# Optimization experiments

Hardware: AMD Instinct MI355X
Metric: run time of the kernel (lower is better)

The kernel has to match this reference:

```python
import jax, jax.numpy as jnp
import numpy as np

B, C, L, NLAB, EMB, NFREQ, D = 256, 64, 512, 10, 256, 9, 8
FIN, FH, FOUT = 4 * C, C, C
P_TOTAL = FIN * FH + FH + FH * FOUT + FOUT + FIN * FOUT + FOUT


def _leaky(x):
    return jax.nn.leaky_relu(x, 0.2)


def _conv1d(x, w, b=None, pad=0):
    y = jax.lax.conv_general_dilated(x, w, (1,), [(pad, pad)], dimension_numbers=('NCH', 'OIH', 'NCH'))
    return y if b is None else y + b[None, :, None]


def _res1d(x, w0, b0, w1, b1, ws=None, pad=1):
    # GAN-stability style residual block: out = shortcut(x) + 0.1 * conv1(act(conv0(act(x))))
    xs = _conv1d(x, ws) if ws is not None else x
    dx = _conv1d(_leaky(x), w0, b0, pad)
    dx = _conv1d(_leaky(dx), w1, b1, pad)
    return xs + 0.1 * dx


def _pos_enc():
    # sinusoidal positional encoding, 2*NFREQ channels over L positions
    p = np.arange(L, dtype=np.float32)
    f = (np.pi / 2.0 ** np.arange(NFREQ, dtype=np.float32))[:, None]
    pe = np.concatenate([np.sin(f * p), np.cos(f * p)], axis=0)  # [2*NFREQ, L]
    return jnp.asarray(pe)


def _sobel_kernels():
    s = np.array([1.0, 2.0, 1.0], np.float32)
    d = np.array([-1.0, 0.0, 1.0], np.float32)
    kx = np.einsum('i,j,k->ijk', d, s, s)
    ky = np.einsum('i,j,k->ijk', s, d, s)
    kz = np.einsum('i,j,k->ijk', s, s, d)
    return jnp.asarray(np.stack([kx, ky, kz]))  # [3, 3, 3, 3]


def _sin_sobel(x, k):
    # depthwise 3D sobel along each axis, sin of gradients, concat with input -> 4C channels
    outs = [x]
    for i in range(3):
        w = jnp.broadcast_to(k[i][None, None], (C, 1, 3, 3, 3))
        g = jax.lax.conv_general_dilated(x, w, (1, 1, 1), [(1, 1)] * 3,
                                         dimension_numbers=('NCDHW', 'OIDHW', 'NCDHW'),
                                         feature_group_count=C)
        outs.append(jnp.sin(g))
    return jnp.concatenate(outs, axis=1)


def _inst_norm(x):
    m = x.mean(axis=(2, 3, 4), keepdims=True)
    v = x.var(axis=(2, 3, 4), keepdims=True)
    return (x - m) * jax.lax.rsqrt(v + 1e-5)


def _dyna(x, p):
    # hypernet-generated per-sample 1x1x1 residual conv block
    b = x.shape[0]
    xf = x.reshape(b, FIN, D * D * D)
    o = FIN * FH
    wh = p[:, :o].reshape(b, FH, FIN)
    bh = p[:, o:o + FH]; o += FH
    wl = p[:, o:o + FH * FOUT].reshape(b, FOUT, FH); o += FH * FOUT
    bl = p[:, o:o + FOUT]; o += FOUT
    ws = p[:, o:o + FIN * FOUT].reshape(b, FOUT, FIN); o += FIN * FOUT
    bs = p[:, o:o + FOUT]
    xs = jnp.einsum('boi,bis->bos', ws, xf) + bs[:, :, None]
    dx = _leaky(jnp.einsum('bhi,bis->bhs', wh, xf) + bh[:, :, None])
    dx = jnp.einsum('boh,bhs->bos', wl, dx) + bl[:, :, None]
    return (xs + 0.1 * dx).reshape(b, FOUT, D, D, D)


def _forward(codes, y, fc_w, fc_b, in_w0, in_b0, in_w1, in_b1, in_ws, leak, hyper_w, hyper_b,
             out_w0, out_b0, out_w1, out_b1, l1_w0, l1_b0, l1_w1, l1_b1,
             l2_w0, l2_b0, l2_w1, l2_b1, l2_ws):
    b = codes.shape[0]
    yemb = jax.nn.one_hot(y, NLAB, dtype=codes.dtype) @ fc_w.T + fc_b
    yemb = yemb / jnp.maximum(jnp.linalg.norm(yemb, axis=1, keepdims=True), 1e-12)
    pe = jnp.broadcast_to(_pos_enc()[None], (b, 2 * NFREQ, L))
    x = jnp.concatenate([codes, pe], axis=1)  # [B, C+2*NFREQ, L]
    x = _res1d(x, in_w0, in_b0, in_w1, in_b1, ws=in_ws)
    x = x.reshape(b, C, D, D, D)
    leak_c = jnp.clip(leak, 0.001, 1000.0)
    p = yemb @ hyper_w.T + hyper_b  # per-sample dynamic conv params [B, P_TOTAL]
    k = _sobel_kernels()
    for _ in range(8):
        xn = _inst_norm(x)
        xn = _sin_sobel(xn, k)
        xn = _dyna(xn, p)
        x = x + leak_c * xn
    x = x.reshape(b, C, L)
    x = _res1d(x, out_w0, out_b0, out_w1, out_b1)
    code_idx = jnp.argmax(codes, axis=1).reshape(b * L)
    logits = x.transpose(0, 2, 1).reshape(b * L, C)
    logp = jax.nn.log_softmax(logits, axis=-1)
    loss_cent = -jnp.take_along_axis(logp, code_idx[:, None], axis=1).mean()
    lat = _res1d(x, l1_w0, l1_b0, l1_w1, l1_b1, pad=0)
    lat = _res1d(lat, l2_w0, l2_b0, l2_w1, l2_b1, ws=l2_ws, pad=0)
    return lat[:, 0, :], loss_cent


def setup_inputs() -> dict:
    key = jax.random.key(0)
    ks = jax.random.split(key, 16)
    w = lambda k, s: 0.02 * jax.random.normal(k, s, jnp.float32)
    z = lambda s: jnp.zeros(s, jnp.float32)
    CIN = C + 2 * NFREQ  # 82
    return {
        'codes': jax.random.normal(ks[0], (B, C, L), jnp.float32),
        'y': jax.random.randint(ks[1], (B,), 0, NLAB),
        'fc_w': w(ks[2], (EMB, NLAB)), 'fc_b': z((EMB,)),
        'in_w0': w(ks[3], (C, CIN, 3)), 'in_b0': z((C,)),
        'in_w1': w(ks[4], (C, C, 3)), 'in_b1': z((C,)),
        'in_ws': w(ks[5], (C, CIN, 1)),
        'leak': jnp.asarray(0.1, jnp.float32),
        'hyper_w': w(ks[6], (P_TOTAL, EMB)), 'hyper_b': z((P_TOTAL,)),
        'out_w0': w(ks[7], (C, C, 3)), 'out_b0': z((C,)),
        'out_w1': w(ks[8], (C, C, 3)), 'out_b1': z((C,)),
        'l1_w0': w(ks[9], (C, C, 1)), 'l1_b0': z((C,)),
        'l1_w1': w(ks[10], (C, C, 1)), 'l1_b1': z((C,)),
        'l2_w0': w(ks[11], (1, C, 1)), 'l2_b0': z((1,)),
        'l2_w1': w(ks[12], (1, 1, 1)), 'l2_b1': z((1,)),
        'l2_ws': w(ks[13], (1, C, 1)),
    }


def reference(codes, y, fc_w, fc_b, in_w0, in_b0, in_w1, in_b1, in_ws, leak, hyper_w, hyper_b,
              out_w0, out_b0, out_w1, out_b1, l1_w0, l1_b0, l1_w1, l1_b1,
              l2_w0, l2_b0, l2_w1, l2_b1, l2_ws):
    return _forward(codes, y, fc_w, fc_b, in_w0, in_b0, in_w1, in_b1, in_ws, leak, hyper_w, hyper_b,
                    out_w0, out_b0, out_w1, out_b1, l1_w0, l1_b0, l1_w1, l1_b1,
                    l2_w0, l2_b0, l2_w1, l2_b1, l2_ws)
```

## Files before the change

### kernel.cpp

```cpp
#include <hip/hip_runtime.h>

#define B_ 256
#define C_ 64
#define L_ 512
#define CIN_ 82
#define NFREQ_ 9
#define EMB_ 256
#define NLAB_ 10
#define PT_ 37056
#define OFF_BH 16384
#define OFF_WL 16448
#define OFF_BL 20544
#define OFF_WS 20608
#define OFF_BS 36992
#define PI_F 3.14159265358979323846f

typedef short bh8 __attribute__((ext_vector_type(8)));
typedef float f32x4 __attribute__((ext_vector_type(4)));

__device__ inline float lrelu(float v){ return v > 0.f ? v : 0.2f*v; }

__device__ inline unsigned short f2bf(float f){
  unsigned u = __float_as_uint(f);
  u += 0x7FFFu + ((u >> 16) & 1u);
  return (unsigned short)(u >> 16);
}
__device__ inline float bf2f(unsigned short u){
  return __uint_as_float((unsigned)u << 16);
}
__device__ inline unsigned pk2(float a, float b){
  return (unsigned)f2bf(a) | ((unsigned)f2bf(b) << 16);
}
__device__ inline bh8 cvt8(float4 a, float4 b){
  bh8 r;
  r[0]=(short)f2bf(a.x); r[1]=(short)f2bf(a.y); r[2]=(short)f2bf(a.z); r[3]=(short)f2bf(a.w);
  r[4]=(short)f2bf(b.x); r[5]=(short)f2bf(b.y); r[6]=(short)f2bf(b.z); r[7]=(short)f2bf(b.w);
  return r;
}
__device__ inline void ld8(const float* p, float* d){
  float4 a = *(const float4*)p, b = *(const float4*)(p + 4);
  d[0]=a.x; d[1]=a.y; d[2]=a.z; d[3]=a.w; d[4]=b.x; d[5]=b.y; d[6]=b.z; d[7]=b.w;
}
__device__ inline void st8(float* p, const float* s){
  float4 a = {s[0],s[1],s[2],s[3]}, b = {s[4],s[5],s[6],s[7]};
  *(float4*)p = a; *(float4*)(p + 4) = b;
}
__device__ inline uint4 pk8(const float* v){
  uint4 o = { pk2(v[0],v[1]), pk2(v[2],v[3]), pk2(v[4],v[5]), pk2(v[6],v[7]) };
  return o;
}

__global__ __launch_bounds__(256) void k_yemb(const float* __restrict__ fc_w,
    const float* __restrict__ fc_b, const int* __restrict__ y,
    unsigned short* __restrict__ ybf, float* __restrict__ out){
  int b = blockIdx.x, e = threadIdx.x;
  int lab = y[b];
  float v = fc_w[e*NLAB_ + lab] + fc_b[e];
  __shared__ float red[256];
  red[e] = v*v; __syncthreads();
  for (int s = 128; s; s >>= 1){ if (e < s) red[e] += red[e+s]; __syncthreads(); }
  float nrm = fmaxf(sqrtf(red[0]), 1e-12f);
  ybf[(size_t)b*EMB_ + e] = f2bf(v / nrm);
  if (b == 0 && e == 0) out[B_*L_] = 0.f;
}

__global__ __launch_bounds__(256) void k_hyper(const float* __restrict__ hw,
    const float* __restrict__ hb, const unsigned short* __restrict__ ybf,
    unsigned short* __restrict__ p_bf){
  int tid = threadIdx.x;
  int wid = tid >> 6, lane = tid & 63, col = lane & 15, quad = lane >> 4;
  int j = blockIdx.x*64 + wid*16 + col;
  f32x4 acc[16];
  f32x4 z4 = {0.f,0.f,0.f,0.f};
  #pragma unroll
  for (int i = 0; i < 16; i++) acc[i] = z4;
  for (int k0 = 0; k0 < 256; k0 += 32){
    const float* hp = hw + (size_t)j*EMB_ + k0 + quad*8;
    bh8 bf = cvt8(*(const float4*)hp, *(const float4*)(hp+4));
    #pragma unroll
    for (int mt = 0; mt < 16; mt++){
      bh8 af = *(const bh8*)&ybf[(size_t)(mt*16 + col)*EMB_ + k0 + quad*8];
      acc[mt] = __builtin_amdgcn_mfma_f32_16x16x32_bf16(af, bf, acc[mt], 0, 0, 0);
    }
  }
  float hbv = hb[j];
  #pragma unroll
  for (int mt = 0; mt < 16; mt++){
    int b0 = mt*16 + quad*4;
    #pragma unroll
    for (int r = 0; r < 4; r++)
      p_bf[(size_t)(b0 + r)*PT_ + j] = f2bf(acc[mt][r] + hbv);
  }
}

__device__ inline float pe_raw(int fi, int l){
  if (fi < NFREQ_) return __sinf(PI_F / (float)(1 << fi) * (float)l);
  return __cosf(PI_F / (float)(1 << (fi - NFREQ_)) * (float)l);
}

__global__ __launch_bounds__(256) void k_conv_in1(const float* __restrict__ codes,
    const float* __restrict__ w0, const float* __restrict__ b0,
    unsigned short* __restrict__ t1bf){
  int b = blockIdx.x, l0 = blockIdx.y*128, tid = threadIdx.x;
  int wid = tid>>6, lane = tid&63, col = lane&15, quad = lane>>4;
  __shared__ __attribute__((aligned(16))) unsigned short xT[136][96];
  __shared__ __attribute__((aligned(16))) unsigned short wA[3][64][96];
  for (int i = tid; i < 64*96; i += 256){
    int m = i / 96, cin = i % 96;
    if (cin < CIN_){
      const float* s = w0 + (size_t)m*(CIN_*3) + cin*3;
      wA[0][m][cin] = f2bf(s[0]); wA[1][m][cin] = f2bf(s[1]); wA[2][m][cin] = f2bf(s[2]);
    } else { wA[0][m][cin] = 0; wA[1][m][cin] = 0; wA[2][m][cin] = 0; }
  }
  const float* cb = codes + (size_t)b*C_*L_;
  for (int i = tid; i < 96*34; i += 256){
    int c = i / 34, g = i % 34;
    int lg = l0 - 4 + 4*g;
    #pragma unroll
    for (int r2 = 0; r2 < 4; r2++){
      int l = lg + r2;
      float xv = 0.f;
      if (l >= 0 && l < L_){
        if (c < C_) xv = cb[(size_t)c*L_ + l];
        else if (c < CIN_) xv = pe_raw(c - C_, l);
      }
      xT[4*g + r2][c] = f2bf(lrelu(xv));
    }
  }
  __syncthreads();
  f32x4 z4 = {0.f,0.f,0.f,0.f};
  f32x4 acc[8];
  #pragma unroll
  for (int i = 0; i < 8; i++) acc[i] = z4;
  #pragma unroll
  for (int t = 0; t < 3; t++){
    #pragma unroll
    for (int k0 = 0; k0 < 96; k0 += 32){
      bh8 bfr[2];
      #pragma unroll
      for (int nt = 0; nt < 2; nt++)
        bfr[nt] = *(const bh8*)&xT[wid*32 + nt*16 + col + t + 3][k0 + quad*8];
      #pragma unroll
      for (int mt = 0; mt < 4; mt++){
        bh8 af = *(const bh8*)&wA[t][mt*16 + col][k0 + quad*8];
        #pragma unroll
        for (int nt = 0; nt < 2; nt++)
          acc[mt*2+nt] = __builtin_amdgcn_mfma_f32_16x16x32_bf16(af, bfr[nt], acc[mt*2+nt], 0,0,0);
      }
    }
  }
  #pragma unroll
  for (int mt = 0; mt < 4; mt++){
    int f0 = mt*16 + quad*4;
    float q0 = b0[f0], q1 = b0[f0+1], q2 = b0[f0+2], q3 = b0[f0+3];
    #pragma unroll
    for (int nt = 0; nt < 2; nt++){
      int l = l0 + wid*32 + nt*16 + col;
      f32x4 a = acc[mt*2+nt];
      uint2 o = { pk2(lrelu(a[0]+q0), lrelu(a[1]+q1)),
                  pk2(lrelu(a[2]+q2), lrelu(a[3]+q3)) };
      *(uint2*)&t1bf[((size_t)b*L_ + l)*64 + f0] = o;
    }
  }
}

__global__ __launch_bounds__(256) void k_conv_in2(const float* __restrict__ codes,
    const float* __restrict__ wsp, const float* __restrict__ w1, const float* __restrict__ b1,
    const unsigned short* __restrict__ t1bf, float* __restrict__ x){
  int b = blockIdx.x, l0 = blockIdx.y*128, tid = threadIdx.x;
  int wid = tid>>6, lane = tid&63, col = lane&15, quad = lane>>4;
  __shared__ __attribute__((aligned(16))) unsigned short xT[128][96];
  __shared__ __attribute__((aligned(16))) unsigned short wsA[64][96];
  __shared__ __attribute__((aligned(16))) unsigned short w1A[3][64][72];
  for (int i = tid; i < 64*96; i += 256){
    int m = i / 96, cin = i % 96;
    wsA[m][cin] = (cin < CIN_) ? f2bf(wsp[(size_t)m*CIN_ + cin]) : (unsigned short)0;
  }
  for (int i = tid; i < 64*64; i += 256){
    int m = i >> 6, cin = i & 63;
    const float* s = w1 + (size_t)m*192 + cin*3;
    w1A[0][m][cin] = f2bf(s[0]); w1A[1][m][cin] = f2bf(s[1]); w1A[2][m][cin] = f2bf(s[2]);
  }
  const float* cb = codes + (size_t)b*C_*L_;
  for (int i = tid; i < 96*32; i += 256){
    int c = i / 32, g = i % 32;
    int lg = l0 + 4*g;
    #pragma unroll
    for (int r2 = 0; r2 < 4; r2++){
      int l = lg + r2;
      float xv;
      if (c < C_) xv = cb[(size_t)c*L_ + l];
      else if (c < CIN_) xv = pe_raw(c - C_, l);
      else xv = 0.f;
      xT[4*g + r2][c] = f2bf(xv);
    }
  }
  __syncthreads();
  f32x4 z4 = {0.f,0.f,0.f,0.f};
  f32x4 accS[8], accD[8];
  #pragma unroll
  for (int i = 0; i < 8; i++){ accS[i] = z4; accD[i] = z4; }
  #pragma unroll
  for (int k0 = 0; k0 < 96; k0 += 32){
    bh8 bfr[2];
    #pragma unroll
    for (int nt = 0; nt < 2; nt++)
      bfr[nt] = *(const bh8*)&xT[wid*32 + nt*16 + col][k0 + quad*8];
    #pragma unroll
    for (int mt = 0; mt < 4; mt++){
      bh8 af = *(const bh8*)&wsA[mt*16 + col][k0 + quad*8];
      #pragma unroll
      for (int nt = 0; nt < 2; nt++)
        accS[mt*2+nt] = __builtin_amdgcn_mfma_f32_16x16x32_bf16(af, bfr[nt], accS[mt*2+nt], 0,0,0);
    }
  }
  bh8 zz8 = {0,0,0,0,0,0,0,0};
  #pragma unroll
  for (int t = 0; t < 3; t++){
    #pragma unroll
    for (int k0 = 0; k0 < 64; k0 += 32){
      bh8 bfr[2];
      #pragma unroll
      for (int nt = 0; nt < 2; nt++){
        int l = l0 + wid*32 + nt*16 + col + t - 1;
        bfr[nt] = (l >= 0 && l < L_)
          ? *(const bh8*)&t1bf[((size_t)b*L_ + l)*64 + k0 + quad*8] : zz8;
      }
      #pragma unroll
      for (int mt = 0; mt < 4; mt++){
        bh8 af = *(const bh8*)&w1A[t][mt*16 + col][k0 + quad*8];
        #pragma unroll
        for (int nt = 0; nt < 2; nt++)
          accD[mt*2+nt] = __builtin_amdgcn_mfma_f32_16x16x32_bf16(af, bfr[nt], accD[mt*2+nt], 0,0,0);
      }
    }
  }
  #pragma unroll
  for (int mt = 0; mt < 4; mt++){
    int f0 = mt*16 + quad*4;
    float q0 = b1[f0], q1 = b1[f0+1], q2 = b1[f0+2], q3 = b1[f0+3];
    #pragma unroll
    for (int nt = 0; nt < 2; nt++){
      int l = l0 + wid*32 + nt*16 + col;
      f32x4 s = accS[mt*2+nt], d = accD[mt*2+nt];
      size_t base = ((size_t)b*C_ + f0)*L_ + l;
      x[base]        = s[0] + 0.1f*(d[0] + q0);
      x[base + L_]   = s[1] + 0.1f*(d[1] + q1);
      x[base + 2*L_] = s[2] + 0.1f*(d[2] + q2);
      x[base + 3*L_] = s[3] + 0.1f*(d[3] + q3);
    }
  }
}

#define TGS 4144
#define TBS (4*TGS)
__global__ __launch_bounds__(512, 2) void k_loop(float* __restrict__ x,
    const unsigned short* __restrict__ p_bf, const float* __restrict__ leak){
  const int b = blockIdx.x, tid = threadIdx.x;
  const int wid = tid >> 6, lane = tid & 63, col = lane & 15, quad = lane >> 4;
  const int yy = lane & 7, zz = lane >> 3;
  const unsigned short* pb = p_bf + (size_t)b*PT_;
  float* xb = x + (size_t)b*C_*L_;

  __shared__ __attribute__((aligned(16))) char sm_raw[81920 + 2*TBS*2];
  float (*S)[64][8] = (float (*)[64][8])(sm_raw + (size_t)wid*(5*64*8*4));
  unsigned short (*h_t)[72] = (unsigned short (*)[72])sm_raw;
  unsigned short* Tb = (unsigned short*)(sm_raw + 81920);

  const int lm = (yy > 0) ? lane-1 : lane;  const float wm = (yy > 0) ? 1.f : 0.f;
  const int lp = (yy < 7) ? lane+1 : lane;  const float wp = (yy < 7) ? 1.f : 0.f;
  const int zm = (zz > 0) ? lane-8 : lane;  const float qm = (zz > 0) ? 1.f : 0.f;
  const int zp = (zz < 7) ? lane+8 : lane;  const float qp = (zz < 7) ? 1.f : 0.f;

  const float lk = fminf(fmaxf(leak[0], 0.001f), 1000.f);
  const int base_t = wid*512 + lane*8;
  const f32x4 z4 = {0.f,0.f,0.f,0.f};

  for (int it = 0; it < 8; ++it){
    f32x4 acc_h[16], acc_s[16];
    #pragma unroll
    for (int i = 0; i < 16; i++){ acc_h[i] = z4; acc_s[i] = z4; }
    const float* xr0 = xb + (size_t)wid*L_ + lane*8;
    float4 nv0 = *(const float4*)xr0, nv1 = *(const float4*)(xr0 + 4);
    for (int cc = 0; cc < 8; ++cc){
      unsigned short* Tc = Tb + (cc & 1)*TBS;
      float r[8] = {nv0.x,nv0.y,nv0.z,nv0.w,nv1.x,nv1.y,nv1.z,nv1.w};
      if (cc < 7){
        const float* xr = xb + (size_t)((cc+1)*8 + wid)*L_ + lane*8;
        nv0 = *(const float4*)xr; nv1 = *(const float4*)(xr + 4);
      }
      float s1 = 0.f, s2 = 0.f;
      #pragma unroll
      for (int i = 0; i < 8; i++){ s1 += r[i]; s2 += r[i]*r[i]; }
      #pragma unroll
      for (int m = 32; m; m >>= 1){ s1 += __shfl_xor(s1, m); s2 += __shfl_xor(s2, m); }
      const float mean = s1 * (1.f/512.f);
      const float rstd = rsqrtf(s2*(1.f/512.f) - mean*mean + 1e-5f);
      float xn[8];
      #pragma unroll
      for (int i = 0; i < 8; i++) xn[i] = (r[i]-mean)*rstd;
      *(uint4*)&Tc[base_t] = pk8(xn);
      float A[8], Bv[8];
      A[0] = 2.f*xn[0]+xn[1]; Bv[0] = xn[1];
      #pragma unroll
      for (int i = 1; i < 7; i++){ A[i] = xn[i-1]+2.f*xn[i]+xn[i+1]; Bv[i] = xn[i+1]-xn[i-1]; }
      A[7] = xn[6]+2.f*xn[7]; Bv[7] = -xn[6];
      st8(&S[0][lane][0], A); st8(&S[1][lane][0], Bv);
      __syncthreads();
      float Cv[8], Dv[8], Ev[8];
      { float am[8], ap[8];
        ld8(&S[0][lm][0], am); ld8(&S[0][lp][0], ap);
        #pragma unroll
        for (int i = 0; i < 8; i++){ float a_m = am[i]*wm, a_p = ap[i]*wp;
          Cv[i] = a_m + 2.f*A[i] + a_p; Dv[i] = a_p - a_m; }
        ld8(&S[1][lm][0], am); ld8(&S[1][lp][0], ap);
        #pragma unroll
        for (int i = 0; i < 8; i++) Ev[i] = am[i]*wm + 2.f*Bv[i] + ap[i]*wp;
      }
      st8(&S[2][lane][0], Cv); st8(&S[3][lane][0], Dv); st8(&S[4][lane][0], Ev);
      __syncthreads();
      { float um[8], up[8], sg[8];
        ld8(&S[2][zm][0], um); ld8(&S[2][zp][0], up);
        #pragma unroll
        for (int i = 0; i < 8; i++) sg[i] = __sinf(up[i]*qp - um[i]*qm);
        *(uint4*)&Tc[TGS + base_t] = pk8(sg);
        ld8(&S[3][zm][0], um); ld8(&S[3][zp][0], up);
        #pragma unroll
        for (int i = 0; i < 8; i++) sg[i] = __sinf(um[i]*qm + 2.f*Dv[i] + up[i]*qp);
        *(uint4*)&Tc[2*TGS + base_t] = pk8(sg);
        ld8(&S[4][zm][0], um); ld8(&S[4][zp][0], up);
        #pragma unroll
        for (int i = 0; i < 8; i++) sg[i] = __sinf(um[i]*qm + 2.f*Ev[i] + up[i]*qp);
        *(uint4*)&Tc[3*TGS + base_t] = pk8(sg);
      }
      __syncthreads();
      bh8 bfr[4];
      #pragma unroll
      for (int nt = 0; nt < 4; nt++){
        const int n = wid*64 + nt*16 + col;
        bh8 fv;
        #pragma unroll
        for (int j = 0; j < 8; j++) fv[j] = (short)Tc[quad*TGS + j*512 + n];
        bfr[nt] = fv;
      }
      #pragma unroll
      for (int mt = 0; mt < 4; mt++){
        const int m = mt*16 + col;
        bh8 ah = *(const bh8*)&pb[(size_t)m*256 + quad*64 + cc*8];
        bh8 aw = *(const bh8*)&pb[OFF_WS + (size_t)m*256 + quad*64 + cc*8];
        #pragma unroll
        for (int nt = 0; nt < 4; nt++){
          acc_h[mt*4+nt] = __builtin_amdgcn_mfma_f32_16x16x32_bf16(ah, bfr[nt], acc_h[mt*4+nt], 0,0,0);
          acc_s[mt*4+nt] = __builtin_amdgcn_mfma_f32_16x16x32_bf16(aw, bfr[nt], acc_s[mt*4+nt], 0,0,0);
        }
      }
    }
    #pragma unroll
    for (int mt = 0; mt < 4; mt++){
      const int f0 = mt*16 + quad*4;
      const float bh0 = bf2f(pb[OFF_BH+f0]),   bh1 = bf2f(pb[OFF_BH+f0+1]);
      const float bh2 = bf2f(pb[OFF_BH+f0+2]), bh3 = bf2f(pb[OFF_BH+f0+3]);
      #pragma unroll
      for (int nt = 0; nt < 4; nt++){
        const int n = wid*64 + nt*16 + col;
        f32x4 a = acc_h[mt*4+nt];
        uint2 o = { pk2(lrelu(a[0]+bh0), lrelu(a[1]+bh1)),
                    pk2(lrelu(a[2]+bh2), lrelu(a[3]+bh3)) };
        *(uint2*)&h_t[n][f0] = o;
      }
    }
    __syncthreads();
    f32x4 acc2[16];
    #pragma unroll
    for (int i = 0; i < 16; i++) acc2[i] = z4;
    #pragma unroll
    for (int k0 = 0; k0 < 64; k0 += 32){
      bh8 hb[4];
      #pragma unroll
      for (int nt = 0; nt < 4; nt++)
        hb[nt] = *(const bh8*)&h_t[wid*64 + nt*16 + col][k0 + quad*8];
      #pragma unroll
      for (int mt = 0; mt < 4; mt++){
        bh8 al = *(const bh8*)&pb[OFF_WL + (size_t)(mt*16 + col)*64 + k0 + quad*8];
        #pragma unroll
        for (int nt = 0; nt < 4; nt++)
          acc2[mt*4+nt] = __builtin_amdgcn_mfma_f32_16x16x32_bf16(al, hb[nt], acc2[mt*4+nt], 0,0,0);
      }
    }
    #pragma unroll
    for (int mt = 0; mt < 4; mt++){
      const int f0 = mt*16 + quad*4;
      const float bs0 = bf2f(pb[OFF_BS+f0]),   bs1 = bf2f(pb[OFF_BS+f0+1]);
      const float bs2 = bf2f(pb[OFF_BS+f0+2]), bs3 = bf2f(pb[OFF_BS+f0+3]);
      const float bl0 = bf2f(pb[OFF_BL+f0]),   bl1 = bf2f(pb[OFF_BL+f0+1]);
      const float bl2 = bf2f(pb[OFF_BL+f0+2]), bl3 = bf2f(pb[OFF_BL+f0+3]);
      #pragma unroll
      for (int nt = 0; nt < 4; nt++){
        const int n = wid*64 + nt*16 + col;
        f32x4 xs = acc_s[mt*4+nt], dx = acc2[mt*4+nt];
        size_t xi = (size_t)f0*L_ + n;
        xb[xi]        += lk*(xs[0] + bs0 + 0.1f*(dx[0] + bl0));
        xb[xi + L_]   += lk*(xs[1] + bs1 + 0.1f*(dx[1] + bl1));
        xb[xi + 2*L_] += lk*(xs[2] + bs2 + 0.1f*(dx[2] + bl2));
        xb[xi + 3*L_] += lk*(xs[3] + bs3 + 0.1f*(dx[3] + bl3));
      }
    }
    __threadfence_block();
    __syncthreads();
  }
}

__global__ __launch_bounds__(256) void k_conv_out1(const float* __restrict__ x,
    const float* __restrict__ w, const float* __restrict__ bias,
    unsigned short* __restrict__ t1bf){
  int b = blockIdx.x, l0 = blockIdx.y*128, tid = threadIdx.x;
  int wid = tid>>6, lane = tid&63, col = lane&15, quad = lane>>4;
  __shared__ __attribute__((aligned(16))) unsigned short xT[136][72];
  __shared__ __attribute__((aligned(16))) unsigned short wA[3][64][72];
  for (int i = tid; i < 64*64; i += 256){
    int m = i >> 6, cin = i & 63;
    const float* s = w + (size_t)m*192 + cin*3;
    wA[0][m][cin] = f2bf(s[0]); wA[1][m][cin] = f2bf(s[1]); wA[2][m][cin] = f2bf(s[2]);
  }
  const float* xb = x + (size_t)b*C_*L_;
  for (int i = tid; i < 64*34; i += 256){
    int c = i / 34, g = i % 34;
    int lg = l0 - 4 + 4*g;
    if (lg >= 0 && lg + 3 < L_){
      float4 f = *(const float4*)&xb[(size_t)c*L_ + lg];
      xT[4*g  ][c] = f2bf(lrelu(f.x));
      xT[4*g+1][c] = f2bf(lrelu(f.y));
      xT[4*g+2][c] = f2bf(lrelu(f.z));
      xT[4*g+3][c] = f2bf(lrelu(f.w));
    } else {
      #pragma unroll
      for (int r2 = 0; r2 < 4; r2++){
        int l = lg + r2;
        float v = (l >= 0 && l < L_) ? xb[(size_t)c*L_ + l] : 0.f;
        xT[4*g + r2][c] = f2bf(lrelu(v));
      }
    }
  }
  __syncthreads();
  f32x4 z4 = {0.f,0.f,0.f,0.f};
  f32x4 acc[8];
  #pragma unroll
  for (int i = 0; i < 8; i++) acc[i] = z4;
  #pragma unroll
  for (int t = 0; t < 3; t++){
    #pragma unroll
    for (int k0 = 0; k0 < 64; k0 += 32){
      bh8 bfr[2];
      #pragma unroll
      for (int nt = 0; nt < 2; nt++)
        bfr[nt] = *(const bh8*)&xT[wid*32 + nt*16 + col + t + 3][k0 + quad*8];
      #pragma unroll
      for (int mt = 0; mt < 4; mt++){
        bh8 af = *(const bh8*)&wA[t][mt*16 + col][k0 + quad*8];
        #pragma unroll
        for (int nt = 0; nt < 2; nt++)
          acc[mt*2+nt] = __builtin_amdgcn_mfma_f32_16x16x32_bf16(af, bfr[nt], acc[mt*2+nt], 0,0,0);
      }
    }
  }
  #pragma unroll
  for (int mt = 0; mt < 4; mt++){
    int f0 = mt*16 + quad*4;
    float q0 = bias[f0], q1 = bias[f0+1], q2 = bias[f0+2], q3 = bias[f0+3];
    #pragma unroll
    for (int nt = 0; nt < 2; nt++){
      int l = l0 + wid*32 + nt*16 + col;
      f32x4 a = acc[mt*2+nt];
      uint2 o = { pk2(lrelu(a[0]+q0), lrelu(a[1]+q1)),
                  pk2(lrelu(a[2]+q2), lrelu(a[3]+q3)) };
      *(uint2*)&t1bf[((size_t)b*L_ + l)*64 + f0] = o;
    }
  }
}

__global__ __launch_bounds__(256) void k_conv_out2(float* __restrict__ x,
    const unsigned short* __restrict__ t1bf, const float* __restrict__ w,
    const float* __restrict__ bias){
  int b = blockIdx.x, l0 = blockIdx.y*256, tid = threadIdx.x;
  int wid = tid>>6, lane = tid&63, col = lane&15, quad = lane>>4;
  __shared__ __attribute__((aligned(16))) unsigned short wA[3][64][72];
  for (int i = tid; i < 64*64; i += 256){
    int m = i >> 6, cin = i & 63;
    const float* s = w + (size_t)m*192 + cin*3;
    wA[0][m][cin] = f2bf(s[0]); wA[1][m][cin] = f2bf(s[1]); wA[2][m][cin] = f2bf(s[2]);
  }
  __syncthreads();
  f32x4 z4 = {0.f,0.f,0.f,0.f};
  f32x4 acc[16];
  #pragma unroll
  for (int i = 0; i < 16; i++) acc[i] = z4;
  bh8 zz8 = {0,0,0,0,0,0,0,0};
  #pragma unroll
  for (int t = 0; t < 3; t++){
    #pragma unroll
    for (int k0 = 0; k0 < 64; k0 += 32){
      bh8 bfr[4];
      #pragma unroll
      for (int nt = 0; nt < 4; nt++){
        int l = l0 + wid*64 + nt*16 + col + t - 1;
        bfr[nt] = (l >= 0 && l < L_)
          ? *(const bh8*)&t1bf[((size_t)b*L_ + l)*64 + k0 + quad*8] : zz8;
      }
      #pragma unroll
      for (int mt = 0; mt < 4; mt++){
        bh8 af = *(const bh8*)&wA[t][mt*16 + col][k0 + quad*8];
        #pragma unroll
        for (int nt = 0; nt < 4; nt++)
          acc[mt*4+nt] = __builtin_amdgcn_mfma_f32_16x16x32_bf16(af, bfr[nt], acc[mt*4+nt], 0,0,0);
      }
    }
  }
  #pragma unroll
  for (int mt = 0; mt < 4; mt++){
    int f0 = mt*16 + quad*4;
    float q0 = bias[f0], q1 = bias[f0+1], q2 = bias[f0+2], q3 = bias[f0+3];
    #pragma unroll
    for (int nt = 0; nt < 4; nt++){
      int l = l0 + wid*64 + nt*16 + col;
      f32x4 a = acc[mt*4+nt];
      size_t base = ((size_t)b*C_ + f0)*L_ + l;
      x[base]        += 0.1f*(a[0] + q0);
      x[base + L_]   += 0.1f*(a[1] + q1);
      x[base + 2*L_] += 0.1f*(a[2] + q2);
      x[base + 3*L_] += 0.1f*(a[3] + q3);
    }
  }
}

__global__ __launch_bounds__(256) void k_loss(const float* __restrict__ x,
    const float* __restrict__ codes, float* __restrict__ out){
  int b = blockIdx.x;
  int l = blockIdx.y*256 + threadIdx.x;
  const float* xb = x + (size_t)b*C_*L_ + l;
  const float* cb = codes + (size_t)b*C_*L_ + l;
  float m = -1e30f, cm = -1e30f;
  int ci = 0;
  for (int c = 0; c < C_; c++){
    float xv = xb[(size_t)c*L_];
    m = fmaxf(m, xv);
    float cv = cb[(size_t)c*L_];
    if (cv > cm){ cm = cv; ci = c; }
  }
  float s = 0.f, vi = 0.f;
  for (int c = 0; c < C_; c++){
    float xv = xb[(size_t)c*L_];
    s += expf(xv - m);
    if (c == ci) vi = xv;
  }
  float lp = vi - m - logf(s);
  __shared__ float red[256];
  red[threadIdx.x] = -lp; __syncthreads();
  for (int sft = 128; sft; sft >>= 1){
    if (threadIdx.x < sft) red[threadIdx.x] += red[threadIdx.x + sft];
    __syncthreads();
  }
  if (threadIdx.x == 0) atomicAdd(out + B_*L_, red[0] * (1.0f/131072.0f));
}

__global__ __launch_bounds__(256) void k_lat(const float* __restrict__ x,
    const float* __restrict__ w10, const float* __restrict__ b10,
    const float* __restrict__ w11, const float* __restrict__ b11,
    const float* __restrict__ w20, const float* __restrict__ b20,
    const float* __restrict__ w21, const float* __restrict__ b21,
    const float* __restrict__ ws2, float* __restrict__ out){
  int b = blockIdx.x, l0 = blockIdx.y*256;
  int tid = threadIdx.x;
  int wid = tid >> 6, lane = tid & 63, col = lane & 15, quad = lane >> 4;
  __shared__ __attribute__((aligned(16))) unsigned short wA[2][64][72];
  __shared__ __attribute__((aligned(16))) unsigned short Bt[256][72];

  for (int i = tid; i < 1024; i += 256){
    int arr = i >> 9, rem = i & 511, row = rem >> 3, seg = rem & 7;
    const float* src = (arr ? w11 : w10) + (size_t)row*C_ + seg*8;
    *(bh8*)&wA[arr][row][seg*8] = cvt8(*(const float4*)src, *(const float4*)(src+4));
  }
  for (int i = tid; i < 4096; i += 256){
    int c = i >> 6, seg = i & 63;
    float4 v = *(const float4*)&x[((size_t)b*C_ + c)*L_ + l0 + seg*4];
    Bt[seg*4+0][c] = f2bf(lrelu(v.x));
    Bt[seg*4+1][c] = f2bf(lrelu(v.y));
    Bt[seg*4+2][c] = f2bf(lrelu(v.z));
    Bt[seg*4+3][c] = f2bf(lrelu(v.w));
  }
  __syncthreads();
  f32x4 z4 = {0.f,0.f,0.f,0.f};
  f32x4 acc1[16];
  #pragma unroll
  for (int i = 0; i < 16; i++) acc1[i] = z4;
  #pragma unroll
  for (int k0 = 0; k0 < 64; k0 += 32){
    bh8 bfr[4];
    #pragma unroll
    for (int nt = 0; nt < 4; nt++)
      bfr[nt] = *(const bh8*)&Bt[wid*64 + nt*16 + col][k0 + quad*8];
    #pragma unroll
    for (int mt = 0; mt < 4; mt++){
      bh8 af = *(const bh8*)&wA[0][mt*16 + col][k0 + quad*8];
      #pragma unroll
      for (int nt = 0; nt < 4; nt++)
        acc1[mt*4+nt] = __builtin_amdgcn_mfma_f32_16x16x32_bf16(af, bfr[nt], acc1[mt*4+nt], 0, 0, 0);
    }
  }
  #pragma unroll
  for (int mt = 0; mt < 4; mt++){
    int f0 = mt*16 + quad*4;
    f32x4 bv = *(const f32x4*)&b10[f0];
    #pragma unroll
    for (int nt = 0; nt < 4; nt++){
      int n = wid*64 + nt*16 + col;
      f32x4 a = acc1[mt*4+nt];
      uint2 o = { pk2(lrelu(a[0]+bv[0]), lrelu(a[1]+bv[1])),
                  pk2(lrelu(a[2]+bv[2]), lrelu(a[3]+bv[3])) };
      *(uint2*)&Bt[n][f0] = o;
    }
  }
  f32x4 acc2[16];
  #pragma unroll
  for (int i = 0; i < 16; i++) acc2[i] = z4;
  #pragma unroll
  for (int k0 = 0; k0 < 64; k0 += 32){
    bh8 bfr[4];
    #pragma unroll
    for (int nt = 0; nt < 4; nt++)
      bfr[nt] = *(const bh8*)&Bt[wid*64 + nt*16 + col][k0 + quad*8];
    #pragma unroll
    for (int mt = 0; mt < 4; mt++){
      bh8 af = *(const bh8*)&wA[1][mt*16 + col][k0 + quad*8];
      #pragma unroll
      for (int nt = 0; nt < 4; nt++)
        acc2[mt*4+nt] = __builtin_amdgcn_mfma_f32_16x16x32_bf16(af, bfr[nt], acc2[mt*4+nt], 0, 0, 0);
    }
  }
  float psA[4] = {0.f,0.f,0.f,0.f}, psB[4] = {0.f,0.f,0.f,0.f};
  #pragma unroll
  for (int mt = 0; mt < 4; mt++){
    int f0 = mt*16 + quad*4;
    f32x4 b11v = *(const f32x4*)&b11[f0];
    f32x4 wsv  = *(const f32x4*)&ws2[f0];
    f32x4 w20v = *(const f32x4*)&w20[f0];
    #pragma unroll
    for (int nt = 0; nt < 4; nt++){
      int lg = l0 + wid*64 + nt*16 + col;
      size_t base = ((size_t)b*C_ + f0)*L_ + lg;
      f32x4 a = acc2[mt*4+nt];
      #pragma unroll
      for (int r = 0; r < 4; r++){
        float xv = x[base + (size_t)r*L_];
        float lat = xv + 0.1f*(a[r] + b11v[r]);
        psA[nt] += wsv[r]*lat;
        psB[nt] += w20v[r]*lrelu(lat);
      }
    }
  }
  #pragma unroll
  for (int nt = 0; nt < 4; nt++){
    psA[nt] += __shfl_xor(psA[nt], 16); psA[nt] += __shfl_xor(psA[nt], 32);
    psB[nt] += __shfl_xor(psB[nt], 16); psB[nt] += __shfl_xor(psB[nt], 32);
  }
  if (quad == 0){
    float b20s = b20[0], w21s = w21[0], b21s = b21[0];
    #pragma unroll
    for (int nt = 0; nt < 4; nt++){
      float dx2 = w21s*lrelu(psB[nt] + b20s) + b21s;
      out[(size_t)b*L_ + l0 + wid*64 + nt*16 + col] = psA[nt] + 0.1f*dx2;
    }
  }
}

extern "C" void kernel_launch(void* const* d_in, const int* in_sizes, int n_in,
                              void* d_out, int out_size, void* d_ws, size_t ws_size,
                              hipStream_t stream) {
  (void)in_sizes; (void)n_in; (void)out_size; (void)ws_size;
  const float* codes   = (const float*)d_in[0];
  const int*   y       = (const int*)  d_in[1];
  const float* fc_w    = (const float*)d_in[2];
  const float* fc_b    = (const float*)d_in[3];
  const float* in_w0   = (const float*)d_in[4];
  const float* in_b0   = (const float*)d_in[5];
  const float* in_w1   = (const float*)d_in[6];
  const float* in_b1   = (const float*)d_in[7];
  const float* in_wsp  = (const float*)d_in[8];
  const float* leak    = (const float*)d_in[9];
  const float* hyper_w = (const float*)d_in[10];
  const float* hyper_b = (const float*)d_in[11];
  const float* out_w0  = (const float*)d_in[12];
  const float* out_b0  = (const float*)d_in[13];
  const float* out_w1  = (const float*)d_in[14];
  const float* out_b1  = (const float*)d_in[15];
  const float* l1_w0   = (const float*)d_in[16];
  const float* l1_b0   = (const float*)d_in[17];
  const float* l1_w1   = (const float*)d_in[18];
  const float* l1_b1   = (const float*)d_in[19];
  const float* l2_w0   = (const float*)d_in[20];
  const float* l2_b0   = (const float*)d_in[21];
  const float* l2_w1   = (const float*)d_in[22];
  const float* l2_b1   = (const float*)d_in[23];
  const float* l2_ws   = (const float*)d_in[24];
  float* out = (float*)d_out;

  char* ws = (char*)d_ws;
  unsigned short* p_bf = (unsigned short*)(ws);
  unsigned short* ybf  = (unsigned short*)(ws + 18972672);
  float* x             = (float*)(ws + 19103744);
  unsigned short* t1bf = (unsigned short*)(ws + 52658176);

  k_yemb<<<B_, 256, 0, stream>>>(fc_w, fc_b, y, ybf, out);
  k_hyper<<<PT_/64, 256, 0, stream>>>(hyper_w, hyper_b, ybf, p_bf);
  k_conv_in1<<<dim3(B_, 4), 256, 0, stream>>>(codes, in_w0, in_b0, t1bf);
  k_conv_in2<<<dim3(B_, 4), 256, 0, stream>>>(codes, in_wsp, in_w1, in_b1, t1bf, x);
  k_loop<<<B_, 512, 0, stream>>>(x, p_bf, leak);
  k_conv_out1<<<dim3(B_, 4), 256, 0, stream>>>(x, out_w0, out_b0, t1bf);
  k_conv_out2<<<dim3(B_, 2), 256, 0, stream>>>(x, t1bf, out_w1, out_b1);
  k_loss<<<dim3(B_, 2), 256, 0, stream>>>(x, codes, out);
  k_lat<<<dim3(B_, 2), 256, 0, stream>>>(x, l1_w0, l1_b0, l1_w1, l1_b1,
                                         l2_w0, l2_b0, l2_w1, l2_b1, l2_ws, out);
}
```

Baseline: 856.6 us.

## Batch 32 channels per sync and use bpermute shuffles for Sobel stencil

In k_loop, the instance-norm and Sobel stage now processes 32 channels per half before one barrier and one MFMA burst, instead of syncing three times per 8-channel chunk. The y/z neighbour exchange for the separable Sobel uses ds_bpermute cross-lane shuffles instead of staging through per-wave shared-memory scratch. The hyper and shortcut accumulators are merged into one 32-tile array, and the barrier after writing h_t is removed because each wave reads only its own rows. The intent is to cut barrier stalls and LDS round-trips. In exchange it issues many more per-dword permutes, and the larger live accumulator set raises register pressure.

```diff
diff --git a/kernel.cpp b/kernel.cpp
--- a/kernel.cpp
+++ b/kernel.cpp
@@ -37,17 +37,12 @@
   r[4]=(short)f2bf(b.x); r[5]=(short)f2bf(b.y); r[6]=(short)f2bf(b.z); r[7]=(short)f2bf(b.w);
   return r;
 }
-__device__ inline void ld8(const float* p, float* d){
-  float4 a = *(const float4*)p, b = *(const float4*)(p + 4);
-  d[0]=a.x; d[1]=a.y; d[2]=a.z; d[3]=a.w; d[4]=b.x; d[5]=b.y; d[6]=b.z; d[7]=b.w;
-}
-__device__ inline void st8(float* p, const float* s){
-  float4 a = {s[0],s[1],s[2],s[3]}, b = {s[4],s[5],s[6],s[7]};
-  *(float4*)p = a; *(float4*)(p + 4) = b;
-}
 __device__ inline uint4 pk8(const float* v){
   uint4 o = { pk2(v[0],v[1]), pk2(v[2],v[3]), pk2(v[4],v[5]), pk2(v[6],v[7]) };
   return o;
+}
+__device__ inline float shf(float v, int a){
+  return __uint_as_float((unsigned)__builtin_amdgcn_ds_bpermute(a, (int)__float_as_uint(v)));
 }
 
 __global__ __launch_bounds__(256) void k_yemb(const float* __restrict__ fc_w,
@@ -252,8 +247,7 @@
   }
 }
 
-#define TGS 4144
-#define TBS (4*TGS)
+#define GSTR 16408
 __global__ __launch_bounds__(512, 2) void k_loop(float* __restrict__ x,
     const unsigned short* __restrict__ p_bf, const float* __restrict__ leak){
   const int b = blockIdx.x, tid = threadIdx.x;
@@ -262,99 +256,96 @@
   const unsigned short* pb = p_bf + (size_t)b*PT_;
   float* xb = x + (size_t)b*C_*L_;
 
-  __shared__ __attribute__((aligned(16))) char sm_raw[81920 + 2*TBS*2];
-  float (*S)[64][8] = (float (*)[64][8])(sm_raw + (size_t)wid*(5*64*8*4));
-  unsigned short (*h_t)[72] = (unsigned short (*)[72])sm_raw;
-  unsigned short* Tb = (unsigned short*)(sm_raw + 81920);
-
-  const int lm = (yy > 0) ? lane-1 : lane;  const float wm = (yy > 0) ? 1.f : 0.f;
-  const int lp = (yy < 7) ? lane+1 : lane;  const float wp = (yy < 7) ? 1.f : 0.f;
-  const int zm = (zz > 0) ? lane-8 : lane;  const float qm = (zz > 0) ? 1.f : 0.f;
-  const int zp = (zz < 7) ? lane+8 : lane;  const float qp = (zz < 7) ? 1.f : 0.f;
+  __shared__ __attribute__((aligned(16))) unsigned short Tbuf[4*GSTR];
+  unsigned short (*h_t)[72] = (unsigned short (*)[72])Tbuf;
+
+  const int lmA = ((yy > 0) ? lane-1 : lane)*4;  const float wm = (yy > 0) ? 1.f : 0.f;
+  const int lpA = ((yy < 7) ? lane+1 : lane)*4;  const float wp = (yy < 7) ? 1.f : 0.f;
+  const int zmA = ((zz > 0) ? lane-8 : lane)*4;  const float qm = (zz > 0) ? 1.f : 0.f;
+  const int zpA = ((zz < 7) ? lane+8 : lane)*4;  const float qp = (zz < 7) ? 1.f : 0.f;
 
   const float lk = fminf(fmaxf(leak[0], 0.001f), 1000.f);
-  const int base_t = wid*512 + lane*8;
   const f32x4 z4 = {0.f,0.f,0.f,0.f};
 
   for (int it = 0; it < 8; ++it){
-    f32x4 acc_h[16], acc_s[16];
-    #pragma unroll
-    for (int i = 0; i < 16; i++){ acc_h[i] = z4; acc_s[i] = z4; }
-    const float* xr0 = xb + (size_t)wid*L_ + lane*8;
-    float4 nv0 = *(const float4*)xr0, nv1 = *(const float4*)(xr0 + 4);
-    for (int cc = 0; cc < 8; ++cc){
-      unsigned short* Tc = Tb + (cc & 1)*TBS;
-      float r[8] = {nv0.x,nv0.y,nv0.z,nv0.w,nv1.x,nv1.y,nv1.z,nv1.w};
-      if (cc < 7){
-        const float* xr = xb + (size_t)((cc+1)*8 + wid)*L_ + lane*8;
-        nv0 = *(const float4*)xr; nv1 = *(const float4*)(xr + 4);
-      }
-      float s1 = 0.f, s2 = 0.f;
-      #pragma unroll
-      for (int i = 0; i < 8; i++){ s1 += r[i]; s2 += r[i]*r[i]; }
-      #pragma unroll
-      for (int m = 32; m; m >>= 1){ s1 += __shfl_xor(s1, m); s2 += __shfl_xor(s2, m); }
-      const float mean = s1 * (1.f/512.f);
-      const float rstd = rsqrtf(s2*(1.f/512.f) - mean*mean + 1e-5f);
-      float xn[8];
-      #pragma unroll
-      for (int i = 0; i < 8; i++) xn[i] = (r[i]-mean)*rstd;
-      *(uint4*)&Tc[base_t] = pk8(xn);
-      float A[8], Bv[8];
-      A[0] = 2.f*xn[0]+xn[1]; Bv[0] = xn[1];
-      #pragma unroll
-      for (int i = 1; i < 7; i++){ A[i] = xn[i-1]+2.f*xn[i]+xn[i+1]; Bv[i] = xn[i+1]-xn[i-1]; }
-      A[7] = xn[6]+2.f*xn[7]; Bv[7] = -xn[6];
-      st8(&S[0][lane][0], A); st8(&S[1][lane][0], Bv);
+    f32x4 acc1[32];
+    #pragma unroll
+    for (int i = 0; i < 32; i++) acc1[i] = z4;
+
+    #pragma unroll 1
+    for (int h = 0; h < 2; ++h){
+      const float* xr0 = xb + (size_t)(h*32 + wid)*L_ + lane*8;
+      float4 nv0 = *(const float4*)xr0, nv1 = *(const float4*)(xr0 + 4);
+      #pragma unroll 1
+      for (int c4 = 0; c4 < 4; ++c4){
+        const int chl = c4*8 + wid;
+        float r[8] = {nv0.x,nv0.y,nv0.z,nv0.w,nv1.x,nv1.y,nv1.z,nv1.w};
+        if (c4 < 3){
+          const float* xr = xb + (size_t)(h*32 + (c4+1)*8 + wid)*L_ + lane*8;
+          nv0 = *(const float4*)xr; nv1 = *(const float4*)(xr + 4);
+        }
+        float s1 = 0.f, s2 = 0.f;
+        #pragma unroll
+        for (int i = 0; i < 8; i++){ s1 += r[i]; s2 += r[i]*r[i]; }
+        #pragma unroll
+        for (int m = 32; m; m >>= 1){ s1 += __shfl_xor(s1, m); s2 += __shfl_xor(s2, m); }
+        const float mean = s1 * (1.f/512.f);
+        const float rstd = rsqrtf(s2*(1.f/512.f) - mean*mean + 1e-5f);
+        float xn[8];
+        #pragma unroll
+        for (int i = 0; i < 8; i++) xn[i] = (r[i]-mean)*rstd;
+        *(uint4*)&Tbuf[chl*512 + lane*8] = pk8(xn);
+        float A[8], Bv[8];
+        A[0] = 2.f*xn[0]+xn[1]; Bv[0] = xn[1];
+        #pragma unroll
+        for (int i = 1; i < 7; i++){ A[i] = xn[i-1]+2.f*xn[i]+xn[i+1]; Bv[i] = xn[i+1]-xn[i-1]; }
+        A[7] = xn[6]+2.f*xn[7]; Bv[7] = -xn[6];
+        float Cv[8], Dv[8], Ev[8];
+        #pragma unroll
+        for (int i = 0; i < 8; i++){
+          float am = shf(A[i], lmA)*wm, ap = shf(A[i], lpA)*wp;
+          Cv[i] = am + 2.f*A[i] + ap;
+          Dv[i] = ap - am;
+          float bm = shf(Bv[i], lmA)*wm, bp = shf(Bv[i], lpA)*wp;
+          Ev[i] = bm + 2.f*Bv[i] + bp;
+        }
+        float g0[8], g1[8], g2[8];
+        #pragma unroll
+        for (int i = 0; i < 8; i++){
+          g0[i] = __sinf(shf(Cv[i], zpA)*qp - shf(Cv[i], zmA)*qm);
+          g1[i] = __sinf(shf(Dv[i], zmA)*qm + 2.f*Dv[i] + shf(Dv[i], zpA)*qp);
+          g2[i] = __sinf(shf(Ev[i], zmA)*qm + 2.f*Ev[i] + shf(Ev[i], zpA)*qp);
+        }
+        *(uint4*)&Tbuf[GSTR   + chl*512 + lane*8] = pk8(g0);
+        *(uint4*)&Tbuf[2*GSTR + chl*512 + lane*8] = pk8(g1);
+        *(uint4*)&Tbuf[3*GSTR + chl*512 + lane*8] = pk8(g2);
+      }
       __syncthreads();
-      float Cv[8], Dv[8], Ev[8];
-      { float am[8], ap[8];
-        ld8(&S[0][lm][0], am); ld8(&S[0][lp][0], ap);
-        #pragma unroll
-        for (int i = 0; i < 8; i++){ float a_m = am[i]*wm, a_p = ap[i]*wp;
-          Cv[i] = a_m + 2.f*A[i] + a_p; Dv[i] = a_p - a_m; }
-        ld8(&S[1][lm][0], am); ld8(&S[1][lp][0], ap);
-        #pragma unroll
-        for (int i = 0; i < 8; i++) Ev[i] = am[i]*wm + 2.f*Bv[i] + ap[i]*wp;
-      }
-      st8(&S[2][lane][0], Cv); st8(&S[3][lane][0], Dv); st8(&S[4][lane][0], Ev);
+      #pragma unroll
+      for (int kt = 0; kt < 4; ++kt){
+        bh8 bfr[4];
+        #pragma unroll
+        for (int nt = 0; nt < 4; nt++){
+          const int n = wid*64 + nt*16 + col;
+          bh8 fv;
+          #pragma unroll
+          for (int j = 0; j < 8; j++) fv[j] = (short)Tbuf[quad*GSTR + (kt*8+j)*512 + n];
+          bfr[nt] = fv;
+        }
+        const int kof = quad*64 + h*32 + kt*8;
+        #pragma unroll
+        for (int mt = 0; mt < 8; mt++){
+          bh8 af = (mt < 4)
+            ? *(const bh8*)&pb[(size_t)(mt*16+col)*256 + kof]
+            : *(const bh8*)&pb[OFF_WS + (size_t)((mt-4)*16+col)*256 + kof];
+          #pragma unroll
+          for (int nt = 0; nt < 4; nt++)
+            acc1[mt*4+nt] = __builtin_amdgcn_mfma_f32_16x16x32_bf16(af, bfr[nt], acc1[mt*4+nt], 0,0,0);
+        }
+      }
       __syncthreads();
-      { float um[8], up[8], sg[8];
-        ld8(&S[2][zm][0], um); ld8(&S[2][zp][0], up);
-        #pragma unroll
-        for (int i = 0; i < 8; i++) sg[i] = __sinf(up[i]*qp - um[i]*qm);
-        *(uint4*)&Tc[TGS + base_t] = pk8(sg);
-        ld8(&S[3][zm][0], um); ld8(&S[3][zp][0], up);
-        #pragma unroll
-        for (int i = 0; i < 8; i++) sg[i] = __sinf(um[i]*qm + 2.f*Dv[i] + up[i]*qp);
-        *(uint4*)&Tc[2*TGS + base_t] = pk8(sg);
-        ld8(&S[4][zm][0], um); ld8(&S[4][zp][0], up);
-        #pragma unroll
-        for (int i = 0; i < 8; i++) sg[i] = __sinf(um[i]*qm + 2.f*Ev[i] + up[i]*qp);
-        *(uint4*)&Tc[3*TGS + base_t] = pk8(sg);
-      }
-      __syncthreads();
-      bh8 bfr[4];
-      #pragma unroll
-      for (int nt = 0; nt < 4; nt++){
-        const int n = wid*64 + nt*16 + col;
-        bh8 fv;
-        #pragma unroll
-        for (int j = 0; j < 8; j++) fv[j] = (short)Tc[quad*TGS + j*512 + n];
-        bfr[nt] = fv;
-      }
-      #pragma unroll
-      for (int mt = 0; mt < 4; mt++){
-        const int m = mt*16 + col;
-        bh8 ah = *(const bh8*)&pb[(size_t)m*256 + quad*64 + cc*8];
-        bh8 aw = *(const bh8*)&pb[OFF_WS + (size_t)m*256 + quad*64 + cc*8];
-        #pragma unroll
-        for (int nt = 0; nt < 4; nt++){
-          acc_h[mt*4+nt] = __builtin_amdgcn_mfma_f32_16x16x32_bf16(ah, bfr[nt], acc_h[mt*4+nt], 0,0,0);
-          acc_s[mt*4+nt] = __builtin_amdgcn_mfma_f32_16x16x32_bf16(aw, bfr[nt], acc_s[mt*4+nt], 0,0,0);
-        }
-      }
-    }
+    }
+
     #pragma unroll
     for (int mt = 0; mt < 4; mt++){
       const int f0 = mt*16 + quad*4;
@@ -363,13 +354,12 @@
       #pragma unroll
       for (int nt = 0; nt < 4; nt++){
         const int n = wid*64 + nt*16 + col;
-        f32x4 a = acc_h[mt*4+nt];
+        f32x4 a = acc1[mt*4+nt];
         uint2 o = { pk2(lrelu(a[0]+bh0), lrelu(a[1]+bh1)),
                     pk2(lrelu(a[2]+bh2), lrelu(a[3]+bh3)) };
         *(uint2*)&h_t[n][f0] = o;
       }
     }
-    __syncthreads();
     f32x4 acc2[16];
     #pragma unroll
     for (int i = 0; i < 16; i++) acc2[i] = z4;
@@ -397,7 +387,7 @@
       #pragma unroll
       for (int nt = 0; nt < 4; nt++){
         const int n = wid*64 + nt*16 + col;
-        f32x4 xs = acc_s[mt*4+nt], dx = acc2[mt*4+nt];
+        f32x4 xs = acc1[(mt+4)*4+nt], dx = acc2[mt*4+nt];
         size_t xi = (size_t)f0*L_ + n;
         xb[xi]        += lk*(xs[0] + bs0 + 0.1f*(dx[0] + bl0));
         xb[xi + L_]   += lk*(xs[1] + bs1 + 0.1f*(dx[1] + bl1));
```

New measurement: 908.8 us. +6.1%, slower.
